# Kernel optimization log

Measured on AMD Instinct MI355X. Metric: run time of the kernel, lower is better.

The kernel has to match this reference:

```python
import jax, jax.numpy as jnp
import numpy as np
import math

NEG = -1e32
B, S, D, H, DFF, L = 16, 512, 1024, 8, 4096, 3
DK = D // H


def layernorm(x, g, b, eps=1e-5):
    mu = x.mean(-1, keepdims=True)
    var = ((x - mu) ** 2).mean(-1, keepdims=True)
    return (x - mu) / jnp.sqrt(var + eps) * g + b


def gen_dam(alphas, E, bmask):
    # alphas, E: [H, S, 2]; hard gumbel-softmax with straight-through
    Hh, Ss, _ = alphas.shape
    g = -jnp.log(E + 1e-5)
    y_soft = jax.nn.softmax(alphas + g, axis=-1)  # tau = 1
    idx = jnp.argmax(y_soft, axis=-1)
    y_hard = jax.nn.one_hot(idx, 2, dtype=y_soft.dtype)
    m = y_hard - jax.lax.stop_gradient(y_soft) + y_soft
    m = jnp.broadcast_to(m[:, :, 0:1], (Hh, Ss, Ss))
    m = jnp.triu(m)
    m = jnp.rot90(m, 1, axes=(1, 2))
    i = jnp.arange(Ss)[:, None]
    j = jnp.arange(Ss)[None, :]
    src = jnp.clip(j - i, 0, Ss - 1)
    shifted = m[:, jnp.arange(Ss)[:, None], src]  # mask_tri[:, i, j] = m[:, i, j - i]
    mask_tri = jnp.where(j >= i, shifted, 0.0)
    masks = mask_tri + jnp.swapaxes(jnp.triu(mask_tri, 1), 1, 2)
    masks = jnp.triu(masks, bmask)
    return masks


def attention(q, k, v, src_mask, dam, zero_pad, gammas):
    # q,k,v: [B,H,S,dk]; src_mask: [S,S] bool; dam: [H,S,S] bool
    dk = q.shape[-1]
    Ss = q.shape[2]
    scores = jnp.einsum('bhqd,bhkd->bhqk', q, k) / math.sqrt(dk)
    damb = dam[None]          # [1,H,S,S]
    smb = src_mask[None, None]  # [1,1,S,S]
    # NOTE: faithful to the torch code, where the first masked_fill(mask==0)
    # result is overwritten - only dam masks the first softmax.
    sc = jnp.where(damb, scores, NEG)
    sc = jax.nn.softmax(sc, axis=-1)
    sc = sc * smb.astype(sc.dtype) * damb.astype(sc.dtype)
    distcum = jnp.cumsum(sc, axis=-1)
    disttot = jnp.sum(sc, axis=-1, keepdims=True)
    pos = jnp.abs(jnp.arange(Ss)[None, :] - jnp.arange(Ss)[:, None]).astype(scores.dtype)
    dist = jnp.sqrt(jnp.clip((disttot - distcum) * pos[None, None], 0.0, None))
    dist = jax.lax.stop_gradient(dist)
    gamma = -jax.nn.softplus(gammas)[None]  # [1,H,1,1]
    te = jnp.clip(jnp.exp(dist * gamma), 1e-5, 1e5)
    scores = scores * te
    scores = jnp.where(smb, scores, NEG)
    scores = jnp.where(damb, scores, NEG)
    scores = jax.nn.softmax(scores, axis=-1)
    if zero_pad:
        scores = scores.at[:, :, 0, :].set(0.0)
    return jnp.einsum('bhqk,bhkd->bhqd', scores, v)


def transformer_layer(bmask, query, key, values, apply_pos, p):
    Bb, Ss, Dd = query.shape
    Hh = p['gammas'].shape[0]
    dam = gen_dam(p['alphas'], p['E'], bmask) == 0
    src_mask = jnp.triu(jnp.ones((Ss, Ss), jnp.int32), bmask) == 0
    k = (key @ p['kW'].T + p['kb']).reshape(Bb, Ss, Hh, -1).transpose(0, 2, 1, 3)
    q = (query @ p['kW'].T + p['kb']).reshape(Bb, Ss, Hh, -1).transpose(0, 2, 1, 3)  # kq_same
    v = (values @ p['vW'].T + p['vb']).reshape(Bb, Ss, Hh, -1).transpose(0, 2, 1, 3)
    att = attention(q, k, v, src_mask, dam, bmask == 0, p['gammas'])
    concat = att.transpose(0, 2, 1, 3).reshape(Bb, Ss, Dd)
    q2 = concat @ p['oW'].T + p['ob']
    x = layernorm(query + q2, p['ln1_g'], p['ln1_b'])
    if apply_pos:
        ff = jax.nn.relu(x @ p['w1'].T + p['b1']) @ p['w2'].T + p['b2']
        x = layernorm(x + ff, p['ln2_g'], p['ln2_b'])
    return x


def setup_inputs() -> dict:
    key = jax.random.key(0)
    ks = jax.random.split(key, 16)
    sc = 0.02
    return {
        'q_embed_data': jax.random.normal(ks[0], (B, S, D), jnp.float32),
        'qa_embed_data': jax.random.normal(ks[1], (B, S, D), jnp.float32),
        'kW': sc * jax.random.normal(ks[2], (L, D, D), jnp.float32),
        'kb': jnp.zeros((L, D), jnp.float32),
        'vW': sc * jax.random.normal(ks[3], (L, D, D), jnp.float32),
        'vb': jnp.zeros((L, D), jnp.float32),
        'oW': sc * jax.random.normal(ks[4], (L, D, D), jnp.float32),
        'ob': jnp.zeros((L, D), jnp.float32),
        'gammas': 0.5 * jax.random.normal(ks[5], (L, H, 1, 1), jnp.float32),
        'alphas': 0.001 * jax.random.normal(ks[6], (L, H, S, 2), jnp.float32),
        'ln1_g': jnp.ones((L, D), jnp.float32),
        'ln1_b': jnp.zeros((L, D), jnp.float32),
        'w1': sc * jax.random.normal(ks[7], (L, DFF, D), jnp.float32),
        'b1': jnp.zeros((L, DFF), jnp.float32),
        'w2': sc * jax.random.normal(ks[8], (L, D, DFF), jnp.float32),
        'b2': jnp.zeros((L, D), jnp.float32),
        'ln2_g': jnp.ones((L, D), jnp.float32),
        'ln2_b': jnp.zeros((L, D), jnp.float32),
        'gumbel_E': jax.random.exponential(ks[9], (L, H, S, 2), jnp.float32),
    }


def reference(q_embed_data, qa_embed_data, kW, kb, vW, vb, oW, ob, gammas,
              alphas, ln1_g, ln1_b, w1, b1, w2, b2, ln2_g, ln2_b, gumbel_E):
    def P(l):
        return {'kW': kW[l], 'kb': kb[l], 'vW': vW[l], 'vb': vb[l],
                'oW': oW[l], 'ob': ob[l], 'gammas': gammas[l], 'alphas': alphas[l],
                'ln1_g': ln1_g[l], 'ln1_b': ln1_b[l], 'w1': w1[l], 'b1': b1[l],
                'w2': w2[l], 'b2': b2[l], 'ln2_g': ln2_g[l], 'ln2_b': ln2_b[l],
                'E': gumbel_E[l]}
    # blocks_1: self-attention over answer embedding (mask=1)
    y = transformer_layer(1, qa_embed_data, qa_embed_data, qa_embed_data, True, P(0))
    # blocks_2: self-attn on question emb (no FFN), then cross-attn into y
    x = transformer_layer(1, q_embed_data, q_embed_data, q_embed_data, False, P(1))
    x = transformer_layer(0, x, x, y, True, P(2))
    return x
```

## Files before the change

### kernel.cpp

```cpp
#include <hip/hip_runtime.h>
#include <math.h>

#define NEGV -1e32f

typedef __bf16 bf16_t;
typedef _Float16 f16_t;
typedef __bf16 bf16x8 __attribute__((ext_vector_type(8)));
typedef __bf16 bf16x4 __attribute__((ext_vector_type(4)));
typedef _Float16 f16x8 __attribute__((ext_vector_type(8)));
typedef float floatx4 __attribute__((ext_vector_type(4)));

static __device__ __forceinline__ float fexp(float x) { return __expf(x); }
#if __has_builtin(__builtin_amdgcn_sqrtf)
static __device__ __forceinline__ float fsqrt(float x) { return __builtin_amdgcn_sqrtf(x); }
#else
static __device__ __forceinline__ float fsqrt(float x) { return sqrtf(x); }
#endif
#if __has_builtin(__builtin_amdgcn_rcpf)
static __device__ __forceinline__ float frcp(float x) { return __builtin_amdgcn_rcpf(x); }
#else
static __device__ __forceinline__ float frcp(float x) { return 1.0f / x; }
#endif

static __device__ __forceinline__ float wave_sum(float v) {
#pragma unroll
  for (int d = 32; d > 0; d >>= 1) v += __shfl_xor(v, d, 64);
  return v;
}
static __device__ __forceinline__ float wave_max(float v) {
#pragma unroll
  for (int d = 32; d > 0; d >>= 1) v = fmaxf(v, __shfl_xor(v, d, 64));
  return v;
}

static __device__ __forceinline__ void gl2lds16(const bf16_t* g, bf16_t* l) {
  __builtin_amdgcn_global_load_lds((__attribute__((address_space(1))) void*)(void*)g,
                                   (__attribute__((address_space(3))) void*)l, 16, 0, 0);
}

template <int WM, int WN, int FM, int FN, int BIAS_MODE, bool RELU, int OUT_MODE>
__global__ __launch_bounds__(WM * WN * 64) void gemm_db(
    const bf16_t* __restrict__ A, long lda, long a_so, long a_si,
    const bf16_t* __restrict__ B, long ldb, long b_so, long b_si,
    void* __restrict__ Cv, long ldc, long c_so, long c_si,
    const float* __restrict__ bias, int zdiv, int K, float alpha)
{
  constexpr int THREADS = WM * WN * 64;
  constexpr int BM = WM * FM * 16;
  constexpr int BN = WN * FN * 16;
  constexpr int RR = THREADS / 8;
  constexpr int RA = BM / RR;
  constexpr int RB = BN / RR;
  constexpr int NSTG = RA + RB;
  constexpr int MG = (FM >= 8) ? 2 : 1;
  constexpr int MSUB = FM / MG;
  constexpr int PH = 2 * MG;
  extern __shared__ bf16_t smem[];
  bf16_t* const Asb = smem;
  bf16_t* const Bsb = smem + 2 * (BM * 64);

  const int tid = threadIdx.x;
  const int wave = tid >> 6;
  const int lane = tid & 63;
  const int wm = wave / WN;
  const int wn = wave % WN;
  const int z = blockIdx.z;
  const long zo = z / zdiv;
  const long zi = z % zdiv;
  A += zo * a_so + zi * a_si;
  B += zo * b_so + zi * b_si;
  const long m0 = (long)blockIdx.x * BM;
  const long n0 = (long)blockIdx.y * BN;

  const int srow = tid >> 3;
  const int scol = ((tid & 7) ^ (srow & 7)) * 8;
  const bf16_t* gA = A + (m0 + srow) * lda + scol;
  const bf16_t* gB = B + (n0 + srow) * ldb + scol;
  const int lofs = wave * 512;

  floatx4 acc[FM][FN] = {};
  const int lr = lane & 15;
  const int kg = lane >> 4;
  const int NT = K >> 6;

  auto stage_round = [&](int q, long ko, int dstbuf) {
    if (q < RA)
      gl2lds16(gA + (long)(q * RR) * lda + ko,
               Asb + dstbuf * (BM * 64) + lofs + q * RR * 64);
    else
      gl2lds16(gB + (long)((q - RA) * RR) * ldb + ko,
               Bsb + dstbuf * (BN * 64) + lofs + (q - RA) * RR * 64);
  };

#pragma unroll
  for (int q = 0; q < NSTG; ++q) stage_round(q, 0, 0);

  for (int t = 0; t < NT; ++t) {
    const int buf = t & 1;
    const bool pf = (t + 1 < NT);
    const long ko = (long)(t + 1) * 64;
    if (pf) {
#pragma unroll
      for (int q = 0; q < 2; ++q) stage_round(q, ko, buf ^ 1);
      asm volatile("s_waitcnt vmcnt(2)" ::: "memory");
    } else {
      asm volatile("s_waitcnt vmcnt(0)" ::: "memory");
    }
    __builtin_amdgcn_s_barrier();
    __builtin_amdgcn_sched_barrier(0);
    const bf16_t* __restrict__ Ab = Asb + buf * (BM * 64);
    const bf16_t* __restrict__ Bb = Bsb + buf * (BN * 64);
#pragma unroll
    for (int h = 0; h < 2; ++h) {
      const int slot = ((h * 4 + kg) ^ (lr & 7)) * 8;
      bf16x8 bfr[FN];
#pragma unroll
      for (int g = 0; g < MG; ++g) {
        const int pi = h * MG + g;
        bf16x8 af[MSUB];
#pragma unroll
        for (int m = 0; m < MSUB; ++m)
          af[m] = *(const bf16x8*)(Ab + (wm * (FM * 16) + (g * MSUB + m) * 16 + lr) * 64 + slot);
        if (g == 0) {
#pragma unroll
          for (int n = 0; n < FN; ++n)
            bfr[n] = *(const bf16x8*)(Bb + (wn * (FN * 16) + n * 16 + lr) * 64 + slot);
        }
        if (pf) {
          const int q0 = 2 + pi * 6 / PH;
          const int q1 = 2 + (pi + 1) * 6 / PH;
#pragma unroll
          for (int q = q0; q < q1; ++q) stage_round(q, ko, buf ^ 1);
        }
        asm volatile("s_waitcnt lgkmcnt(0)" ::: "memory");
        __builtin_amdgcn_sched_barrier(0);
        __builtin_amdgcn_s_setprio(1);
#pragma unroll
        for (int m = 0; m < MSUB; ++m)
#pragma unroll
          for (int n = 0; n < FN; ++n)
            acc[g * MSUB + m][n] =
                __builtin_amdgcn_mfma_f32_16x16x32_bf16(af[m], bfr[n], acc[g * MSUB + m][n], 0, 0, 0);
        __builtin_amdgcn_s_setprio(0);
        __builtin_amdgcn_sched_barrier(0);
        __builtin_amdgcn_s_barrier();
      }
    }
  }

  const long coff = zo * c_so + zi * c_si;
  const int q4 = (lane >> 4) * 4;
#pragma unroll
  for (int m = 0; m < FM; ++m) {
#pragma unroll
    for (int n = 0; n < FN; ++n) {
#pragma unroll
      for (int r = 0; r < 4; ++r) {
        const long row = m0 + wm * (FM * 16) + m * 16 + q4 + r;
        const long col = n0 + wn * (FN * 16) + n * 16 + lr;
        float v = acc[m][n][r] * alpha;
        if (BIAS_MODE == 1) v += bias[col];
        if (BIAS_MODE == 2) v += bias[row];
        if (RELU) v = fmaxf(v, 0.0f);
        const long idx = coff + row * ldc + col;
        if (OUT_MODE == 1)      ((bf16_t*)Cv)[idx] = (bf16_t)v;
        else if (OUT_MODE == 2) ((f16_t*)Cv)[idx]  = (f16_t)v;
        else                    ((float*)Cv)[idx]  = v;
      }
    }
  }
}

__global__ __launch_bounds__(256, 3) void attn_fused(
    const bf16_t* __restrict__ KQ,
    const bf16_t* __restrict__ VT,
    bf16_t* __restrict__ ATT,
    const int* __restrict__ bbit_l, const float* __restrict__ gam,
    const int bmask, const int zero_pad)
{
  __shared__ f16_t Sp16[32 * 512];
  bf16_t* const SpB = (bf16_t*)Sp16;

  const int tid = threadIdx.x;
  const int wave = tid >> 6;
  const int lane = tid & 63;
  const int lr = lane & 15;
  const int kg = lane >> 4;
  const int id = blockIdx.x;
  const int wg = (id & 7) * 256 + (id >> 3);
  const int bh = wg >> 4;
  const int qb = wg & 15;
  const int b = bh >> 3, h = bh & 7;
  const bf16_t* Qp = KQ + (long)b * 524288 + h * 128 + (long)qb * 32 * 1024;
  const bf16_t* Kp = KQ + (long)b * 524288 + h * 128;
  const bf16_t* Vp = VT + (long)b * 524288 + (long)h * 65536;

  floatx4 acc[2][8] = {};
  bf16x8 aq[2][2][2];
#pragma unroll
  for (int kt = 0; kt < 2; ++kt)
#pragma unroll
    for (int hh = 0; hh < 2; ++hh)
#pragma unroll
      for (int m = 0; m < 2; ++m)
        aq[kt][hh][m] =
            *(const bf16x8*)(Qp + (long)(m * 16 + lr) * 1024 + kt * 64 + (hh * 4 + kg) * 8);

#pragma unroll
  for (int step = 0; step < 4; ++step) {
    const int kt = step >> 1;
    const int hb = step & 1;
#pragma unroll
    for (int hh = 0; hh < 2; ++hh) {
      bf16x8 bfr[4];
#pragma unroll
      for (int n = 0; n < 4; ++n)
        bfr[n] = *(const bf16x8*)(Kp + (long)(hb * 256 + wave * 64 + n * 16 + lr) * 1024 +
                                  kt * 64 + (hh * 4 + kg) * 8);
#pragma unroll
      for (int m = 0; m < 2; ++m)
#pragma unroll
        for (int n = 0; n < 4; ++n)
          acc[m][hb * 4 + n] =
              __builtin_amdgcn_mfma_f32_16x16x32_bf16(aq[kt][hh][m], bfr[n], acc[m][hb * 4 + n], 0, 0, 0);
    }
    __builtin_amdgcn_sched_barrier(0);
  }

  const int q4 = kg * 4;
#pragma unroll
  for (int m = 0; m < 2; ++m)
#pragma unroll
    for (int na = 0; na < 8; ++na)
#pragma unroll
      for (int rr = 0; rr < 4; ++rr) {
        const int row = m * 16 + q4 + rr;
        const int col = (na >> 2) * 256 + wave * 64 + (na & 3) * 16 + lr;
        const int g = (col >> 3) ^ (row & 7);
        Sp16[row * 512 + g * 8 + (col & 7)] = (f16_t)(acc[m][na][rr] * 0.08838834764831845f);
      }
  __syncthreads();

  {
    const float gamma = -log1pf(fexp(gam[h]));
    const int* bb = bbit_l + h * 512;
#pragma unroll 1
    for (int rr8 = 0; rr8 < 8; ++rr8) {
      const int r = wave * 8 + rr8;
      const int i = qb * 32 + r;
      const int jb = lane * 8;
      const int ga = r * 512 + ((lane ^ (r & 7)) << 3);
      float sv[8];
      {
        const f16x8 a = *(const f16x8*)(Sp16 + ga);
#pragma unroll
        for (int u = 0; u < 8; ++u) sv[u] = (float)a[u];
      }
      float zz[8];
      bool band[8];
      float m1 = NEGV;
#pragma unroll
      for (int u = 0; u < 8; ++u) {
        const int j = jb + u;
        const bool bd = j < i + bmask;
        band[u] = bd;
        int d = j - i; d = d < 0 ? 0 : d;
        const bool allowed = bd || (bb[d] == 0);
        zz[u] = allowed ? sv[u] : NEGV;
        m1 = fmaxf(m1, zz[u]);
      }
      m1 = wave_max(m1);
      float e[8], es = 0.f;
#pragma unroll
      for (int u = 0; u < 8; ++u) { e[u] = fexp(zz[u] - m1); es += e[u]; }
      es = wave_sum(es);
      const float inv1 = frcp(es);
      float c[8];
      float run = 0.f;
#pragma unroll
      for (int u = 0; u < 8; ++u) {
        const float p = band[u] ? e[u] * inv1 : 0.f;
        run += p;
        c[u] = run;
      }
      float x = run;
#pragma unroll
      for (int d = 1; d < 64; d <<= 1) {
        const float y = __shfl_up(x, (unsigned)d, 64);
        if (lane >= d) x += y;
      }
      const float tot = __shfl(x, 63, 64);
      const float ex = x - run;
      float z2[8];
      float m2 = NEGV;
#pragma unroll
      for (int u = 0; u < 8; ++u) {
        const int j = jb + u;
        const float cc = c[u] + ex;
        const float pos = fabsf((float)(i - j));
        const float dist = fsqrt(fmaxf((tot - cc) * pos, 0.f));
        float te = fexp(dist * gamma);
        te = fminf(fmaxf(te, 1e-5f), 1e5f);
        z2[u] = band[u] ? sv[u] * te : NEGV;
        m2 = fmaxf(m2, z2[u]);
      }
      m2 = wave_max(m2);
      float f[8], es2 = 0.f;
#pragma unroll
      for (int u = 0; u < 8; ++u) { f[u] = fexp(z2[u] - m2); es2 += f[u]; }
      es2 = wave_sum(es2);
      const float inv2 = (zero_pad && i == 0) ? 0.f : frcp(es2);
      bf16x8 o;
#pragma unroll
      for (int u = 0; u < 8; ++u) o[u] = (bf16_t)(f[u] * inv2);
      *(bf16x8*)(SpB + ga) = o;
    }
  }
  __syncthreads();

  floatx4 acc2[2][2] = {};
#pragma unroll 1
  for (int kt = 0; kt < 8; ++kt) {
#pragma unroll
    for (int hh = 0; hh < 2; ++hh) {
      const int ks = hh * 4 + kg;
      bf16x8 af[2], bfr[2];
#pragma unroll
      for (int m = 0; m < 2; ++m) {
        const int row = m * 16 + lr;
        const int g = (kt * 8 + ks) ^ (lr & 7);
        af[m] = *(const bf16x8*)(SpB + row * 512 + g * 8);
      }
#pragma unroll
      for (int n = 0; n < 2; ++n)
        bfr[n] = *(const bf16x8*)(Vp + (long)(wave * 32 + n * 16 + lr) * 512 +
                                  kt * 64 + ks * 8);
#pragma unroll
      for (int m = 0; m < 2; ++m)
#pragma unroll
        for (int n = 0; n < 2; ++n)
          acc2[m][n] = __builtin_amdgcn_mfma_f32_16x16x32_bf16(af[m], bfr[n], acc2[m][n], 0, 0, 0);
    }
  }

#pragma unroll
  for (int m = 0; m < 2; ++m)
#pragma unroll
    for (int n = 0; n < 2; ++n)
#pragma unroll
      for (int rr = 0; rr < 4; ++rr) {
        const int row = m * 16 + q4 + rr;
        const int col = wave * 32 + n * 16 + lr;
        ATT[(long)b * 524288 + (long)(qb * 32 + row) * 1024 + h * 128 + col] =
            (bf16_t)acc2[m][n][rr];
      }
}

__global__ __launch_bounds__(256) void cast_kernel(const float* __restrict__ in,
                                                   bf16_t* __restrict__ out, long n)
{
  const long i = ((long)blockIdx.x * 256 + threadIdx.x) * 4;
  if (i >= n) return;
  const float4 v = *(const float4*)(in + i);
  bf16x4 o;
  o[0] = (bf16_t)v.x; o[1] = (bf16_t)v.y; o[2] = (bf16_t)v.z; o[3] = (bf16_t)v.w;
  *(bf16x4*)(out + i) = o;
}

__global__ void bbit_kernel(const float* __restrict__ alphas, const float* __restrict__ E,
                            int* __restrict__ bbit, int n)
{
  const int i = blockIdx.x * 256 + threadIdx.x;
  if (i >= n) return;
  const float l0 = alphas[2 * i]     - logf(E[2 * i]     + 1e-5f);
  const float l1 = alphas[2 * i + 1] - logf(E[2 * i + 1] + 1e-5f);
  bbit[i] = (l0 >= l1) ? 1 : 0;
}

template <bool XBF>
__global__ __launch_bounds__(256) void ln_kernel(
    const void* __restrict__ Xv, const float* __restrict__ R,
    const float* __restrict__ g, const float* __restrict__ b,
    float* __restrict__ out32, bf16_t* __restrict__ out16)
{
  const long row = blockIdx.x;
  const int t = threadIdx.x;
  float x0, x1, x2, x3;
  if (XBF) {
    const bf16x4 xv = *(const bf16x4*)((const bf16_t*)Xv + row * 1024 + t * 4);
    x0 = (float)xv[0]; x1 = (float)xv[1]; x2 = (float)xv[2]; x3 = (float)xv[3];
  } else {
    const float4 xv = *(const float4*)((const float*)Xv + row * 1024 + t * 4);
    x0 = xv.x; x1 = xv.y; x2 = xv.z; x3 = xv.w;
  }
  const float4 rv = *(const float4*)(R + row * 1024 + t * 4);
  const float v0 = x0 + rv.x, v1 = x1 + rv.y, v2 = x2 + rv.z, v3 = x3 + rv.w;
  float s  = v0 + v1 + v2 + v3;
  float s2 = v0 * v0 + v1 * v1 + v2 * v2 + v3 * v3;
  s = wave_sum(s); s2 = wave_sum(s2);
  __shared__ float red[8];
  const int wv = t >> 6, lane = t & 63;
  if (lane == 0) { red[wv] = s; red[4 + wv] = s2; }
  __syncthreads();
  s  = red[0] + red[1] + red[2] + red[3];
  s2 = red[4] + red[5] + red[6] + red[7];
  const float mu = s * (1.0f / 1024.0f);
  const float var = s2 * (1.0f / 1024.0f) - mu * mu;
  const float rstd = rsqrtf(var + 1e-5f);
  const float4 gv = *(const float4*)(g + t * 4);
  const float4 bv = *(const float4*)(b + t * 4);
  float4 ov;
  ov.x = (v0 - mu) * rstd * gv.x + bv.x;
  ov.y = (v1 - mu) * rstd * gv.y + bv.y;
  ov.z = (v2 - mu) * rstd * gv.z + bv.z;
  ov.w = (v3 - mu) * rstd * gv.w + bv.w;
  if (out32) *(float4*)(out32 + row * 1024 + t * 4) = ov;
  if (out16) {
    bf16x4 oh;
    oh[0] = (bf16_t)ov.x; oh[1] = (bf16_t)ov.y; oh[2] = (bf16_t)ov.z; oh[3] = (bf16_t)ov.w;
    *(bf16x4*)(out16 + row * 1024 + t * 4) = oh;
  }
}

extern "C" void kernel_launch(void* const* d_in, const int* in_sizes, int n_in,
                              void* d_out, int out_size, void* d_ws, size_t ws_size,
                              hipStream_t stream)
{
  (void)in_sizes; (void)n_in; (void)out_size; (void)ws_size;
  const float* q_emb  = (const float*)d_in[0];
  const float* qa_emb = (const float*)d_in[1];
  const float* kW = (const float*)d_in[2];
  const float* kb = (const float*)d_in[3];
  const float* vW = (const float*)d_in[4];
  const float* vb = (const float*)d_in[5];
  const float* oW = (const float*)d_in[6];
  const float* ob = (const float*)d_in[7];
  const float* gammas = (const float*)d_in[8];
  const float* alphas = (const float*)d_in[9];
  const float* ln1_g = (const float*)d_in[10];
  const float* ln1_b = (const float*)d_in[11];
  const float* w1 = (const float*)d_in[12];
  const float* b1 = (const float*)d_in[13];
  const float* w2 = (const float*)d_in[14];
  const float* b2 = (const float*)d_in[15];
  const float* ln2_g = (const float*)d_in[16];
  const float* ln2_b = (const float*)d_in[17];
  const float* gumE = (const float*)d_in[18];
  float* outp = (float*)d_out;

  static bool attr_done = false;
  if (!attr_done) {
    attr_done = true;
    (void)hipFuncSetAttribute(reinterpret_cast<const void*>(&gemm_db<2,2,4,4,1,false,1>),
                              hipFuncAttributeMaxDynamicSharedMemorySize, 65536);
    (void)hipFuncSetAttribute(reinterpret_cast<const void*>(&gemm_db<2,2,4,4,2,false,1>),
                              hipFuncAttributeMaxDynamicSharedMemorySize, 65536);
    (void)hipFuncSetAttribute(reinterpret_cast<const void*>(&gemm_db<2,2,4,4,1,false,0>),
                              hipFuncAttributeMaxDynamicSharedMemorySize, 65536);
    (void)hipFuncSetAttribute(reinterpret_cast<const void*>(&gemm_db<2,4,8,4,1,true,1>),
                              hipFuncAttributeMaxDynamicSharedMemorySize, 131072);
  }

  const size_t MBc = 1ull << 20;
  char* W = (char*)d_ws;
  int*    bbit = (int*)W;
  bf16_t* VB   = (bf16_t*)(W + 1 * MBc);
  bf16_t* XB   = (bf16_t*)(W + 17 * MBc);
  bf16_t* kWb  = (bf16_t*)(W + 33 * MBc);
  bf16_t* vWb  = (bf16_t*)(W + 39 * MBc);
  bf16_t* oWb  = (bf16_t*)(W + 45 * MBc);
  bf16_t* w1b  = (bf16_t*)(W + 51 * MBc);
  bf16_t* w2b  = (bf16_t*)(W + 59 * MBc);
  bf16_t* KQB  = (bf16_t*)(W + 67 * MBc);
  bf16_t* VT   = (bf16_t*)(W + 83 * MBc);
  bf16_t* ATT  = (bf16_t*)(W + 163 * MBc);
  float*  O32  = (float*)(W + 67 * MBc);
  bf16_t* X1B  = (bf16_t*)(W + 99 * MBc);
  bf16_t* H1B  = (bf16_t*)(W + 115 * MBc);

  const long ND = 8388608;

  auto run_layer = [&](int l, const void* Qin, bool qin_bf16, const bf16_t* XBp,
                       const bf16_t* VBp, bool apply_pos, int bmask,
                       float* o32, bf16_t* o16) {
    const bf16_t* kWl = kWb + (long)l * 1048576;
    const bf16_t* vWl = vWb + (long)l * 1048576;
    const bf16_t* oWl = oWb + (long)l * 1048576;
    gemm_db<2,2,4,4,1,false,1><<<dim3(64, 8, 1), dim3(256), 65536, stream>>>(
        XBp, 1024, 0, 0, kWl, 1024, 0, 0, (void*)KQB, 1024, 0, 0,
        kb + l * 1024, 1, 1024, 1.0f);
    gemm_db<2,2,4,4,2,false,1><<<dim3(8, 4, 16), dim3(256), 65536, stream>>>(
        vWl, 1024, 0, 0, VBp, 1024, 524288, 0, (void*)VT, 512, 524288, 0,
        vb + l * 1024, 1, 1024, 1.0f);
    const int zp = (bmask == 0) ? 1 : 0;
    attn_fused<<<dim3(2048), dim3(256), 0, stream>>>(
        KQB, VT, ATT, bbit + l * 4096, gammas + l * 8, bmask, zp);
    gemm_db<2,2,4,4,1,false,0><<<dim3(64, 8, 1), dim3(256), 65536, stream>>>(
        ATT, 1024, 0, 0, oWl, 1024, 0, 0, (void*)O32, 1024, 0, 0,
        ob + l * 1024, 1, 1024, 1.0f);
    if (!apply_pos) {
      if (qin_bf16)
        ln_kernel<true><<<dim3(8192), dim3(256), 0, stream>>>(
            Qin, O32, ln1_g + l * 1024, ln1_b + l * 1024, o32, o16);
      else
        ln_kernel<false><<<dim3(8192), dim3(256), 0, stream>>>(
            Qin, O32, ln1_g + l * 1024, ln1_b + l * 1024, o32, o16);
    } else {
      cast_kernel<<<dim3(4096), dim3(256), 0, stream>>>(w1 + (long)l * 4194304, w1b, 4194304);
      cast_kernel<<<dim3(4096), dim3(256), 0, stream>>>(w2 + (long)l * 4194304, w2b, 4194304);
      if (qin_bf16)
        ln_kernel<true><<<dim3(8192), dim3(256), 0, stream>>>(
            Qin, O32, ln1_g + l * 1024, ln1_b + l * 1024, nullptr, X1B);
      else
        ln_kernel<false><<<dim3(8192), dim3(256), 0, stream>>>(
            Qin, O32, ln1_g + l * 1024, ln1_b + l * 1024, nullptr, X1B);
      gemm_db<2,4,8,4,1,true,1><<<dim3(32, 16, 1), dim3(512), 131072, stream>>>(
          X1B, 1024, 0, 0, w1b, 1024, 0, 0, (void*)H1B, 4096, 0, 0,
          b1 + l * 4096, 1, 1024, 1.0f);
      gemm_db<2,2,4,4,1,false,0><<<dim3(64, 8, 1), dim3(256), 65536, stream>>>(
          H1B, 4096, 0, 0, w2b, 4096, 0, 0, (void*)O32, 1024, 0, 0,
          b2 + l * 1024, 1, 4096, 1.0f);
      ln_kernel<true><<<dim3(8192), dim3(256), 0, stream>>>(
          X1B, O32, ln2_g + l * 1024, ln2_b + l * 1024, o32, o16);
    }
  };

  bbit_kernel<<<dim3(48), dim3(256), 0, stream>>>(alphas, gumE, bbit, 12288);
  cast_kernel<<<dim3(3072), dim3(256), 0, stream>>>(kW, kWb, 3145728);
  cast_kernel<<<dim3(3072), dim3(256), 0, stream>>>(vW, vWb, 3145728);
  cast_kernel<<<dim3(3072), dim3(256), 0, stream>>>(oW, oWb, 3145728);

  cast_kernel<<<dim3(8192), dim3(256), 0, stream>>>(qa_emb, XB, ND);
  run_layer(0, qa_emb, false, XB, XB, true, 1, nullptr, VB);
  cast_kernel<<<dim3(8192), dim3(256), 0, stream>>>(q_emb, XB, ND);
  run_layer(1, q_emb, false, XB, XB, false, 1, nullptr, XB);
  run_layer(2, XB, true, XB, VB, true, 0, outp, nullptr);
}
```

Baseline: 1.173 ms.

## Split attention work across eight waves per block instead of four

The fused attention kernel now runs 512 threads (8 waves) per block. Each wave computes a 64-key slice of the QK^T scores, handles 4 softmax rows instead of 8, and produces a 16-column slice of the PV output. The goal is shorter per-wave serial work, fewer registers per wave, and more latency hiding within a block. In exchange, Q fragments are reloaded by more waves, each wave issues fewer MFMAs, and the launch bound requests 8 blocks per CU. That target may be limited by the 32KB of shared memory each block uses.

```diff
diff --git a/kernel.cpp b/kernel.cpp
--- a/kernel.cpp
+++ b/kernel.cpp
@@ -171,7 +171,7 @@
   }
 }
 
-__global__ __launch_bounds__(256, 3) void attn_fused(
+__global__ __launch_bounds__(512, 8) void attn_fused(
     const bf16_t* __restrict__ KQ,
     const bf16_t* __restrict__ VT,
     bf16_t* __restrict__ ATT,
@@ -195,49 +195,39 @@
   const bf16_t* Kp = KQ + (long)b * 524288 + h * 128;
   const bf16_t* Vp = VT + (long)b * 524288 + (long)h * 65536;
 
-  floatx4 acc[2][8] = {};
-  bf16x8 aq[2][2][2];
-#pragma unroll
-  for (int kt = 0; kt < 2; ++kt)
-#pragma unroll
-    for (int hh = 0; hh < 2; ++hh)
+  const int kb0 = wave * 64;
+  floatx4 acc[2][4] = {};
+#pragma unroll
+  for (int kt = 0; kt < 2; ++kt) {
+#pragma unroll
+    for (int hh = 0; hh < 2; ++hh) {
+      const int co = kt * 64 + (hh * 4 + kg) * 8;
+      bf16x8 aq[2], bfr[4];
 #pragma unroll
       for (int m = 0; m < 2; ++m)
-        aq[kt][hh][m] =
-            *(const bf16x8*)(Qp + (long)(m * 16 + lr) * 1024 + kt * 64 + (hh * 4 + kg) * 8);
-
-#pragma unroll
-  for (int step = 0; step < 4; ++step) {
-    const int kt = step >> 1;
-    const int hb = step & 1;
-#pragma unroll
-    for (int hh = 0; hh < 2; ++hh) {
-      bf16x8 bfr[4];
+        aq[m] = *(const bf16x8*)(Qp + (long)(m * 16 + lr) * 1024 + co);
 #pragma unroll
       for (int n = 0; n < 4; ++n)
-        bfr[n] = *(const bf16x8*)(Kp + (long)(hb * 256 + wave * 64 + n * 16 + lr) * 1024 +
-                                  kt * 64 + (hh * 4 + kg) * 8);
+        bfr[n] = *(const bf16x8*)(Kp + (long)(kb0 + n * 16 + lr) * 1024 + co);
 #pragma unroll
       for (int m = 0; m < 2; ++m)
 #pragma unroll
         for (int n = 0; n < 4; ++n)
-          acc[m][hb * 4 + n] =
-              __builtin_amdgcn_mfma_f32_16x16x32_bf16(aq[kt][hh][m], bfr[n], acc[m][hb * 4 + n], 0, 0, 0);
-    }
-    __builtin_amdgcn_sched_barrier(0);
+          acc[m][n] = __builtin_amdgcn_mfma_f32_16x16x32_bf16(aq[m], bfr[n], acc[m][n], 0, 0, 0);
+    }
   }
 
   const int q4 = kg * 4;
 #pragma unroll
   for (int m = 0; m < 2; ++m)
 #pragma unroll
-    for (int na = 0; na < 8; ++na)
+    for (int n = 0; n < 4; ++n)
 #pragma unroll
       for (int rr = 0; rr < 4; ++rr) {
         const int row = m * 16 + q4 + rr;
-        const int col = (na >> 2) * 256 + wave * 64 + (na & 3) * 16 + lr;
+        const int col = kb0 + n * 16 + lr;
         const int g = (col >> 3) ^ (row & 7);
-        Sp16[row * 512 + g * 8 + (col & 7)] = (f16_t)(acc[m][na][rr] * 0.08838834764831845f);
+        Sp16[row * 512 + g * 8 + (col & 7)] = (f16_t)(acc[m][n][rr] * 0.08838834764831845f);
       }
   __syncthreads();
 
@@ -245,8 +235,8 @@
     const float gamma = -log1pf(fexp(gam[h]));
     const int* bb = bbit_l + h * 512;
 #pragma unroll 1
-    for (int rr8 = 0; rr8 < 8; ++rr8) {
-      const int r = wave * 8 + rr8;
+    for (int rr4 = 0; rr4 < 4; ++rr4) {
+      const int r = wave * 4 + rr4;
       const int i = qb * 32 + r;
       const int jb = lane * 8;
       const int ga = r * 512 + ((lane ^ (r & 7)) << 3);
@@ -318,42 +308,34 @@
   }
   __syncthreads();
 
-  floatx4 acc2[2][2] = {};
+  floatx4 acc2[2] = {};
 #pragma unroll 1
   for (int kt = 0; kt < 8; ++kt) {
 #pragma unroll
     for (int hh = 0; hh < 2; ++hh) {
       const int ks = hh * 4 + kg;
-      bf16x8 af[2], bfr[2];
+      bf16x8 af[2], bfr;
 #pragma unroll
       for (int m = 0; m < 2; ++m) {
-        const int row = m * 16 + lr;
         const int g = (kt * 8 + ks) ^ (lr & 7);
-        af[m] = *(const bf16x8*)(SpB + row * 512 + g * 8);
-      }
-#pragma unroll
-      for (int n = 0; n < 2; ++n)
-        bfr[n] = *(const bf16x8*)(Vp + (long)(wave * 32 + n * 16 + lr) * 512 +
-                                  kt * 64 + ks * 8);
+        af[m] = *(const bf16x8*)(SpB + (m * 16 + lr) * 512 + g * 8);
+      }
+      bfr = *(const bf16x8*)(Vp + (long)(wave * 16 + lr) * 512 + kt * 64 + ks * 8);
 #pragma unroll
       for (int m = 0; m < 2; ++m)
-#pragma unroll
-        for (int n = 0; n < 2; ++n)
-          acc2[m][n] = __builtin_amdgcn_mfma_f32_16x16x32_bf16(af[m], bfr[n], acc2[m][n], 0, 0, 0);
+        acc2[m] = __builtin_amdgcn_mfma_f32_16x16x32_bf16(af[m], bfr, acc2[m], 0, 0, 0);
     }
   }
 
 #pragma unroll
   for (int m = 0; m < 2; ++m)
 #pragma unroll
-    for (int n = 0; n < 2; ++n)
-#pragma unroll
-      for (int rr = 0; rr < 4; ++rr) {
-        const int row = m * 16 + q4 + rr;
-        const int col = wave * 32 + n * 16 + lr;
-        ATT[(long)b * 524288 + (long)(qb * 32 + row) * 1024 + h * 128 + col] =
-            (bf16_t)acc2[m][n][rr];
-      }
+    for (int rr = 0; rr < 4; ++rr) {
+      const int row = m * 16 + q4 + rr;
+      const int col = wave * 16 + lr;
+      ATT[(long)b * 524288 + (long)(qb * 32 + row) * 1024 + h * 128 + col] =
+          (bf16_t)acc2[m][rr];
+    }
 }
 
 __global__ __launch_bounds__(256) void cast_kernel(const float* __restrict__ in,
@@ -493,7 +475,7 @@
         vWl, 1024, 0, 0, VBp, 1024, 524288, 0, (void*)VT, 512, 524288, 0,
         vb + l * 1024, 1, 1024, 1.0f);
     const int zp = (bmask == 0) ? 1 : 0;
-    attn_fused<<<dim3(2048), dim3(256), 0, stream>>>(
+    attn_fused<<<dim3(2048), dim3(512), 0, stream>>>(
         KQB, VT, ATT, bbit + l * 4096, gammas + l * 8, bmask, zp);
     gemm_db<2,2,4,4,1,false,0><<<dim3(64, 8, 1), dim3(256), 65536, stream>>>(
         ATT, 1024, 0, 0, oWl, 1024, 0, 0, (void*)O32, 1024, 0, 0,
```

Result: slower. 1.246 ms (+6.2%).
